# Kernel tuning notes

Hardware: AMD Instinct MI355X
Metric: run time of the kernel (lower is better)

The kernel has to match this reference:

```python
import jax, jax.numpy as jnp
import numpy as np

B, T, C, H = 8, 2048, 1024, 16
N_LAYER, LAYER_ID = 12, 1
NH = C // H           # head size = 64
CHUNK = 256


def setup_inputs() -> dict:
    key = jax.random.key(0)
    ks = jax.random.split(key, 10)
    # deterministic init matching the torch __init__
    ratio_0_to_1 = LAYER_ID / (N_LAYER - 1)
    ratio_1_to_almost0 = 1.0 - LAYER_ID / N_LAYER
    ddd = np.arange(C, dtype=np.float32) / C
    time_maa_k = (1.0 - ddd ** ratio_1_to_almost0).astype(np.float32)
    time_maa_v = (1.0 - (ddd ** ratio_1_to_almost0 + 0.3 * ratio_0_to_1)).astype(np.float32)
    time_maa_r = (1.0 - ddd ** (0.5 * ratio_1_to_almost0)).astype(np.float32)
    h_idx = np.arange(H, dtype=np.float32)
    time_decay = (-6.0 + 5.0 * (h_idx / (H - 1)) ** (0.7 + 1.3 * ratio_0_to_1)).astype(np.float32)
    s = 0.02
    return {
        "x": jax.random.normal(ks[0], (B, T, C), jnp.float32),
        "volatility": jax.random.uniform(ks[1], (B, T), jnp.float32),
        "Wvol": jax.random.normal(ks[2], (C, 1), jnp.float32) * s,
        "bvol": jnp.zeros((C,), jnp.float32),
        "time_maa_k": jnp.asarray(time_maa_k),
        "time_maa_v": jnp.asarray(time_maa_v),
        "time_maa_r": jnp.asarray(time_maa_r),
        "time_decay": jnp.asarray(time_decay),
        "Wk": jax.random.normal(ks[3], (C, C), jnp.float32) * s,
        "Wv": jax.random.normal(ks[4], (C, C), jnp.float32) * s,
        "Wr": jax.random.normal(ks[5], (C, C), jnp.float32) * s,
        "Wo": jax.random.normal(ks[6], (C, C), jnp.float32) * s,
        "gn_w": 1.0 + jax.random.normal(ks[7], (C,), jnp.float32) * s,
        "gn_b": jax.random.normal(ks[8], (C,), jnp.float32) * s,
    }


def reference(x, volatility, Wvol, bvol, time_maa_k, time_maa_v, time_maa_r,
              time_decay, Wk, Wv, Wr, Wo, gn_w, gn_b):
    b, t, c = x.shape
    h = time_decay.shape[0]
    n = c // h
    nc = t // CHUNK

    # volatility gating: sigmoid(Linear(1->C))
    v_emb = jax.nn.sigmoid(volatility[:, :, None] * Wvol[:, 0] + bvol)  # (B,T,C)
    x = x * v_emb

    # time shift (zero-pad one step at the front, drop last)
    xx = jnp.pad(x, ((0, 0), (1, 0), (0, 0)))[:, :-1] - x
    xk = x + xx * time_maa_k
    xv = x + xx * time_maa_v
    xr = x + xx * time_maa_r

    r = (xr @ Wr.T).reshape(b, t, h, n).transpose(0, 2, 1, 3)  # (B,H,T,N)
    k = (xk @ Wk.T).reshape(b, t, h, n).transpose(0, 2, 1, 3)
    v = (xv @ Wv.T).reshape(b, t, h, n).transpose(0, 2, 1, 3)

    w = jnp.exp(-jnp.exp(time_decay))[None, :, None, None]  # scalar decay per head

    # chunked linear-attention recurrence (faithful to torch loop, chunk=256, no intra-chunk mask)
    rc = r.reshape(b, h, nc, CHUNK, n).transpose(2, 0, 1, 3, 4)  # (nc,B,H,CK,N)
    kc = k.reshape(b, h, nc, CHUNK, n).transpose(2, 0, 1, 3, 4)
    vc = v.reshape(b, h, nc, CHUNK, n).transpose(2, 0, 1, 3, 4)

    def step(state, rkv):
        rr, kk, vv = rkv  # each (B,H,CK,N)
        att = jnp.einsum('bhtn,bhsn->bhts', rr, kk)            # r @ k^T
        y = w * (jnp.einsum('bhts,bhsn->bhtn', att, vv)
                 + jnp.einsum('bhtn,bhnm->bhtm', rr, state))
        new_state = w * (state + jnp.einsum('bhsn,bhsm->bhnm', kk, vv))
        return new_state, y

    state0 = jnp.zeros((b, h, n, n), x.dtype)
    _, ys = jax.lax.scan(step, state0, (rc, kc, vc))            # (nc,B,H,CK,N)
    y = ys.transpose(1, 2, 0, 3, 4).reshape(b, h, t, n)
    y = y.transpose(0, 2, 1, 3).reshape(b * t, c)

    # GroupNorm with H groups over channels
    yg = y.reshape(b * t, h, n)
    mu = yg.mean(-1, keepdims=True)
    var = yg.var(-1, keepdims=True)
    yg = (yg - mu) * jax.lax.rsqrt(var + 1e-5)
    y = (yg.reshape(b * t, c) * gn_w + gn_b).reshape(b, t, c)

    return y @ Wo.T  # dropout is identity in eval
```

## Files before the change

### kernel.cpp

```cpp
#include <hip/hip_runtime.h>

typedef unsigned short u16;
typedef __attribute__((ext_vector_type(4))) unsigned int u32x4;
typedef __attribute__((ext_vector_type(4))) float f32x4;
typedef __attribute__((ext_vector_type(8))) short s16x8;

#define B_ 8
#define T_ 2048
#define C_ 1024
#define H_ 16
#define HS_ 64
#define CHUNK_ 256
#define NC_ 8

union U8 { u32x4 u; u16 h[8]; };

__device__ __forceinline__ float b2f(u16 v) {
    union { unsigned int i; float f; } c; c.i = ((unsigned int)v) << 16; return c.f;
}
__device__ __forceinline__ u16 f2b(float f) {
    union { float f; unsigned int i; } c; c.f = f;
    unsigned int i = c.i;
    return (u16)((i + 0x7FFFu + ((i >> 16) & 1u)) >> 16);
}
__device__ __forceinline__ float fsig(float z) {
    return __builtin_amdgcn_rcpf(1.f + __expf(-z));
}

typedef __attribute__((address_space(1))) void GV;
typedef __attribute__((address_space(3))) void LV;
__device__ __forceinline__ void glds16(const void* g, void* l) {
    __builtin_amdgcn_global_load_lds((GV*)g, (LV*)l, 16, 0, 0);
}

__global__ __launch_bounds__(256) void cvt4_kernel(
    const float* __restrict__ s0, const float* __restrict__ s1,
    const float* __restrict__ s2, const float* __restrict__ s3,
    u16* __restrict__ dst)
{
    int i = blockIdx.x * 256 + threadIdx.x;
    int m = i >> 17;
    const float* s = (m == 0) ? s0 : (m == 1) ? s1 : (m == 2) ? s2 : s3;
    size_t j = (size_t)(i & 131071) * 8;
    f32x4 a = *reinterpret_cast<const f32x4*>(s + j);
    f32x4 b = *reinterpret_cast<const f32x4*>(s + j + 4);
    U8 o;
    #pragma unroll
    for (int k = 0; k < 4; k++) { o.h[k] = f2b(a[k]); o.h[4 + k] = f2b(b[k]); }
    *reinterpret_cast<u32x4*>(dst + (size_t)m * C_ * C_ + j) = o.u;
}

__global__ __launch_bounds__(256) void mix_kernel(
    const float* __restrict__ x, const float* __restrict__ vol,
    const float* __restrict__ Wvol, const float* __restrict__ bvol,
    const float* __restrict__ mk, const float* __restrict__ mv, const float* __restrict__ mr,
    u16* __restrict__ xk, u16* __restrict__ xv, u16* __restrict__ xr)
{
    int idx = blockIdx.x * 256 + threadIdx.x;
    int c0 = (idx & 127) * 8;
    int bt4 = idx >> 7;
    int t0  = (bt4 & 511) * 4;
    int b   = bt4 >> 9;
    size_t rowOff = ((size_t)b * T_ + t0) * C_ + c0;

    float wv[8], bv[8], mkv[8], mvv[8], mrv[8];
    #pragma unroll
    for (int j = 0; j < 8; j += 4) {
        f32x4 a;
        a = *reinterpret_cast<const f32x4*>(Wvol + c0 + j);
        wv[j] = a[0]; wv[j+1] = a[1]; wv[j+2] = a[2]; wv[j+3] = a[3];
        a = *reinterpret_cast<const f32x4*>(bvol + c0 + j);
        bv[j] = a[0]; bv[j+1] = a[1]; bv[j+2] = a[2]; bv[j+3] = a[3];
        a = *reinterpret_cast<const f32x4*>(mk + c0 + j);
        mkv[j] = a[0]; mkv[j+1] = a[1]; mkv[j+2] = a[2]; mkv[j+3] = a[3];
        a = *reinterpret_cast<const f32x4*>(mv + c0 + j);
        mvv[j] = a[0]; mvv[j+1] = a[1]; mvv[j+2] = a[2]; mvv[j+3] = a[3];
        a = *reinterpret_cast<const f32x4*>(mr + c0 + j);
        mrv[j] = a[0]; mrv[j+1] = a[1]; mrv[j+2] = a[2]; mrv[j+3] = a[3];
    }

    const float* volb = vol + (size_t)b * T_;
    float gp[8];
    if (t0 == 0) {
        #pragma unroll
        for (int j = 0; j < 8; j++) gp[j] = 0.f;
    } else {
        float vp = volb[t0 - 1];
        #pragma unroll
        for (int j = 0; j < 8; j += 4) {
            f32x4 a = *reinterpret_cast<const f32x4*>(x + rowOff - C_ + j);
            gp[j]   = a[0] * fsig(vp * wv[j]   + bv[j]);
            gp[j+1] = a[1] * fsig(vp * wv[j+1] + bv[j+1]);
            gp[j+2] = a[2] * fsig(vp * wv[j+2] + bv[j+2]);
            gp[j+3] = a[3] * fsig(vp * wv[j+3] + bv[j+3]);
        }
    }

    #pragma unroll
    for (int s = 0; s < 4; s++) {
        float vc = volb[t0 + s];
        size_t off = rowOff + (size_t)s * C_;
        float g[8];
        #pragma unroll
        for (int j = 0; j < 8; j += 4) {
            f32x4 a = *reinterpret_cast<const f32x4*>(x + off + j);
            g[j]   = a[0] * fsig(vc * wv[j]   + bv[j]);
            g[j+1] = a[1] * fsig(vc * wv[j+1] + bv[j+1]);
            g[j+2] = a[2] * fsig(vc * wv[j+2] + bv[j+2]);
            g[j+3] = a[3] * fsig(vc * wv[j+3] + bv[j+3]);
        }
        U8 ok, ov, orr;
        #pragma unroll
        for (int j = 0; j < 8; j++) {
            float xx = gp[j] - g[j];
            ok.h[j]  = f2b(g[j] + xx * mkv[j]);
            ov.h[j]  = f2b(g[j] + xx * mvv[j]);
            orr.h[j] = f2b(g[j] + xx * mrv[j]);
            gp[j] = g[j];
        }
        *reinterpret_cast<u32x4*>(xk + off) = ok.u;
        *reinterpret_cast<u32x4*>(xv + off) = ov.u;
        *reinterpret_cast<u32x4*>(xr + off) = orr.u;
    }
}

#define GBM_ 256
#define GBN_ 256
#define GBK_ 64
#define GK_  1024
#define GNT_ 16
#define GEMM_LDS_BYTES 131072

template<int MODE>
__global__ __launch_bounds__(512, 2) void gemm_bt(
    const u16* __restrict__ A, const u16* __restrict__ W, void* __restrict__ Cc)
{
    extern __shared__ __align__(16) u16 lds[];
    const int tid  = threadIdx.x;
    const int lane = tid & 63, w = tid >> 6;
    const int r16  = lane & 15, quad = lane >> 4;
    const int wm2  = w >> 2;
    const int wn4  = w & 3;
    const int id   = blockIdx.x;
    const int bm   = id & 63, bn = id >> 6;

    const u16* Ab = A + (size_t)bm * GBM_ * GK_;
    const u16* Wb = W + (size_t)bn * GBN_ * GK_;

    const int srow8  = lane >> 3;
    const int schunk = ((lane & 7) ^ srow8) * 8;
    const u16* aSrc  = Ab + (size_t)(w * 16 + srow8) * GK_ + schunk;
    const u16* bSrcR = Wb + (size_t)srow8 * GK_ + schunk;

    const int fA0 = (wm2 * 128 + r16) * 64;
    const int fB0 = 16384 + (wn4 * 64 + r16) * 64;
    const int c0 = ((quad)     ^ (r16 & 7)) * 8;
    const int c1 = ((quad | 4) ^ (r16 & 7)) * 8;

    const int i0_ = w * 2, i1_ = w * 2 + 1;
    const int rB0 = (i0_ >> 2) * 64 + (i0_ & 3) * 8;
    const int rB1 = (i1_ >> 2) * 64 + (i1_ & 3) * 8;

    f32x4 acc[8][4];
    #pragma unroll
    for (int mi = 0; mi < 8; mi++)
        #pragma unroll
        for (int ni = 0; ni < 4; ni++)
            acc[mi][ni] = f32x4{0.f, 0.f, 0.f, 0.f};

#define SQA(tt) do {                                                          \
    const size_t ko_ = (size_t)(tt) * 64;                                     \
    u16* db_ = lds + (((tt) & 1) * 32768) + w * 1024;                         \
    glds16(aSrc + ko_,                 db_);                                  \
    glds16(aSrc + 8   * GK_ + ko_,     db_ + 512);                            \
    glds16(aSrc + 128 * GK_ + ko_,     db_ + 8192);                           \
    glds16(aSrc + 136 * GK_ + ko_,     db_ + 8192 + 512);                     \
} while (0)

#define SQB(tt, hi) do {                                                      \
    const size_t ko_ = (size_t)(tt) * 64;                                     \
    u16* bb_ = lds + (((tt) & 1) * 32768) + 16384;                            \
    const int ra_ = rB0 + (hi) * 32, rb_ = rB1 + (hi) * 32;                   \
    glds16(bSrcR + (size_t)ra_ * GK_ + ko_, bb_ + ra_ * 64);                  \
    glds16(bSrcR + (size_t)rb_ * GK_ + ko_, bb_ + rb_ * 64);                  \
} while (0)

#define PH_BAR() do { asm volatile("" ::: "memory");                          \
    __builtin_amdgcn_s_barrier(); asm volatile("" ::: "memory"); } while (0)
#define PH_LGKM0() do { asm volatile("s_waitcnt lgkmcnt(0)" ::: "memory");    \
    __builtin_amdgcn_sched_barrier(0); } while (0)
#define LDFA(CO) { _Pragma("unroll") for (int mi = 0; mi < 8; mi++)           \
    fa[mi] = *reinterpret_cast<const s16x8*>(lds + pb + fA0 + mi * 1024 + (CO)); }
#define LDFB(NH, CO) { _Pragma("unroll") for (int ni = 0; ni < 2; ni++)       \
    fb[ni] = *reinterpret_cast<const s16x8*>(lds + pb + fB0 + ((NH) * 2 + ni) * 1024 + (CO)); }
#define MFMA16(NH) do { __builtin_amdgcn_s_setprio(1);                        \
    _Pragma("unroll") for (int mi = 0; mi < 8; mi++) {                        \
        acc[mi][(NH)*2+0] = __builtin_amdgcn_mfma_f32_16x16x32_bf16(          \
            fa[mi], fb[0], acc[mi][(NH)*2+0], 0, 0, 0);                       \
        acc[mi][(NH)*2+1] = __builtin_amdgcn_mfma_f32_16x16x32_bf16(          \
            fa[mi], fb[1], acc[mi][(NH)*2+1], 0, 0, 0);                       \
    } __builtin_amdgcn_s_setprio(0); } while (0)

    SQA(0); SQB(0, 0); SQB(0, 1);

    for (int t = 0; t < GNT_; ++t) {
        const int pb = (t & 1) * 32768;
        s16x8 fa[8], fb[2];
        asm volatile("s_waitcnt vmcnt(2)" ::: "memory");
        PH_BAR();
        LDFA(c0); LDFB(0, c0);
        if (t + 1 < GNT_) SQA(t + 1);
        PH_LGKM0(); MFMA16(0);
        if (t + 1 < GNT_) asm volatile("s_waitcnt vmcnt(4)" ::: "memory");
        else              asm volatile("s_waitcnt vmcnt(0)" ::: "memory");
        PH_BAR();
        LDFB(1, c0);
        if (t + 1 < GNT_) SQB(t + 1, 0);
        PH_LGKM0(); MFMA16(1);
        LDFA(c1); LDFB(0, c1);
        PH_BAR();
        if (t + 1 < GNT_) SQB(t + 1, 1);
        PH_LGKM0(); MFMA16(0);
        LDFB(1, c1);
        PH_BAR();
        PH_LGKM0(); MFMA16(1);
    }
#undef SQA
#undef SQB
#undef LDFA
#undef LDFB
#undef MFMA16
#undef PH_LGKM0
#undef PH_BAR

    asm volatile("s_waitcnt vmcnt(0)" ::: "memory");
    __builtin_amdgcn_s_barrier();
    asm volatile("" ::: "memory");

    if constexpr (MODE == 0) {
        float* C = (float*)Cc;
        #pragma unroll
        for (int mi = 0; mi < 8; mi++) {
            int row0 = bm * GBM_ + wm2 * 128 + mi * 16 + quad * 4;
            #pragma unroll
            for (int ni = 0; ni < 4; ni++) {
                int col = bn * GBN_ + wn4 * 64 + ni * 16 + r16;
                #pragma unroll
                for (int i = 0; i < 4; i++)
                    C[(size_t)(row0 + i) * C_ + col] = acc[mi][ni][i];
            }
        }
    } else if constexpr (MODE == 1) {
        u16* ep = lds + w * 4608;
        u16* C = (u16*)Cc;
        #pragma unroll
        for (int half = 0; half < 2; half++) {
            #pragma unroll
            for (int mi2 = 0; mi2 < 4; mi2++) {
                int mi = half * 4 + mi2;
                #pragma unroll
                for (int ni = 0; ni < 4; ni++)
                    #pragma unroll
                    for (int i = 0; i < 4; i++)
                        ep[(mi2 * 16 + quad * 4 + i) * 72 + ni * 16 + r16] =
                            f2b(acc[mi][ni][i]);
            }
            asm volatile("s_waitcnt lgkmcnt(0)" ::: "memory");
            __builtin_amdgcn_sched_barrier(0);
            #pragma unroll
            for (int it = 0; it < 8; it++) {
                int rr = it * 8 + (lane >> 3);
                u32x4 val = *reinterpret_cast<const u32x4*>(ep + rr * 72 + (lane & 7) * 8);
                size_t grow = (size_t)(bm * GBM_ + wm2 * 128 + half * 64 + rr);
                *reinterpret_cast<u32x4*>(
                    C + grow * C_ + bn * GBN_ + wn4 * 64 + (lane & 7) * 8) = val;
            }
            asm volatile("s_waitcnt vmcnt(0) lgkmcnt(0)" ::: "memory");
        }
    } else {
        u16* ep = lds + w * 8192;
        #pragma unroll
        for (int mi = 0; mi < 8; mi++) {
            const int chunk = mi * 2 + (quad >> 1);
            const int rsub = (quad & 1) * 4;
            #pragma unroll
            for (int ni = 0; ni < 4; ni++) {
                const int col = ni * 16 + r16;
                u16* p = ep + col * 128 + ((chunk ^ col) & 15) * 8 + rsub;
                p[0] = f2b(acc[mi][ni][0]);
                p[1] = f2b(acc[mi][ni][1]);
                p[2] = f2b(acc[mi][ni][2]);
                p[3] = f2b(acc[mi][ni][3]);
            }
        }
        asm volatile("s_waitcnt lgkmcnt(0)" ::: "memory");
        __builtin_amdgcn_sched_barrier(0);
        u16* C = (u16*)Cc;
        const int cl = lane >> 2, ch4 = lane & 3;
        const int gc0 = bn * 16 + wn4 * 4;
        const int tt0 = bm * 8 + wm2 * 4;
        #pragma unroll
        for (int it = 0; it < 16; it++) {
            const int col_l = (it & 3) * 16 + cl;
            const int chunk = (it >> 2) * 4 + ch4;
            u32x4 val = *reinterpret_cast<const u32x4*>(
                ep + col_l * 128 + ((chunk ^ col_l) & 15) * 8);
            const size_t tile = (size_t)(gc0 + (it & 3)) * 512 + tt0 + (it >> 2);
            *reinterpret_cast<u32x4*>(C + tile * 512 + cl * 32 + ch4 * 8) = val;
        }
    }
}

#define KVS_LDS_BYTES 98304

__global__ __launch_bounds__(512) void kvscan_kernel(
    const u16* __restrict__ kT, const u16* __restrict__ vT,
    const float* __restrict__ td, u16* __restrict__ stT)
{
    extern __shared__ __align__(16) u16 klds[];
    const int bm2 = blockIdx.x;
    const int mh = bm2 & 1, bh = bm2 >> 1;
    const int h = bh & (H_ - 1), b = bh >> 4;
    const float wdec = expf(-expf(td[h]));
    const int tid = threadIdx.x, lane = tid & 63, w = tid >> 6;
    const int r16 = lane & 15, quad = lane >> 4;
    const int cgn = w >> 1;
    const int ck  = w & 1;
    const int tt0 = b * 64;
    const int loff = r16 * 32 + quad * 8;

#define KSTG(jj, bb) do {                                                     \
    u16* db_ = klds + (bb) * 24576;                                           \
    _Pragma("unroll")                                                         \
    for (int q = 0; q < 6; q++) {                                             \
        const int tau = w * 6 + q;                                            \
        const u16* src;                                                       \
        if (tau < 32)                                                         \
            src = vT + ((size_t)(h * 4 + (tau >> 3)) * 512 +                  \
                        tt0 + (jj) * 8 + (tau & 7)) * 512;                    \
        else                                                                  \
            src = kT + ((size_t)(h * 4 + mh * 2 + ((tau - 32) >> 3)) * 512 +  \
                        tt0 + (jj) * 8 + ((tau - 32) & 7)) * 512;             \
        glds16(src + (size_t)lane * 8, db_ + tau * 512);                      \
    }                                                                         \
} while (0)

    KSTG(0, 0);

    f32x4 st = f32x4{0.f, 0.f, 0.f, 0.f};
    for (int j = 0; j < NC_; ++j) {
        asm volatile("s_waitcnt vmcnt(0)" ::: "memory");
        __syncthreads();
        if (j + 1 < NC_) KSTG(j + 1, (j + 1) & 1);
        const u16* bb = klds + (j & 1) * 24576;
        f32x4 acc = f32x4{0.f, 0.f, 0.f, 0.f};
        #pragma unroll
        for (int ks = 0; ks < 8; ks++) {
            s16x8 fa = *reinterpret_cast<const s16x8*>(
                bb + (cgn * 8 + ks) * 512 + loff);
            s16x8 fb = *reinterpret_cast<const s16x8*>(
                bb + (32 + ck * 8 + ks) * 512 + loff);
            acc = __builtin_amdgcn_mfma_f32_16x16x32_bf16(fa, fb, acc, 0, 0, 0);
        }
        st = (st + acc) * wdec;
        u16* out = stT + ((size_t)bh * NC_ + j) * 4096;
        #pragma unroll
        for (int i = 0; i < 4; i++)
            out[(cgn * 16 + quad * 4 + i) * HS_ + mh * 32 + ck * 16 + r16] =
                f2b(st[i]);
    }
#undef KSTG
}

__global__ __launch_bounds__(256) void rstate_gn_kernel(
    const u16* __restrict__ r, const u16* __restrict__ stT,
    const float* __restrict__ gnw, const float* __restrict__ gnb, u16* __restrict__ ygn)
{
    int blk = blockIdx.x;
    int c  = blk & (NC_ - 1);
    int bh = blk >> 3;
    int h = bh & (H_ - 1);
    int b = bh >> 4;
    __shared__ __align__(16) u16 sT[HS_ * 72];
    int tid = threadIdx.x, lane = tid & 63, wave = tid >> 6;
    int r16 = lane & 15, quad = lane >> 4;

    const u16* sg = stT + (size_t)blk * (HS_ * HS_);
    for (int i = tid; i < 512; i += 256) {
        int n = i >> 3, c8 = (i & 7) * 8;
        *reinterpret_cast<u32x4*>(&sT[n * 72 + c8]) =
            *reinterpret_cast<const u32x4*>(sg + n * HS_ + c8);
    }
    __syncthreads();

    size_t rowBase = (size_t)(b * T_ + c * CHUNK_ + wave * 64);
    f32x4 acc[4][4];
    #pragma unroll
    for (int mi = 0; mi < 4; mi++)
        #pragma unroll
        for (int ni = 0; ni < 4; ni++)
            acc[mi][ni] = f32x4{0.f, 0.f, 0.f, 0.f};

    #pragma unroll
    for (int ks = 0; ks < 2; ks++) {
        int kb = ks * 32 + quad * 8;
        s16x8 fa[4], fb[4];
        #pragma unroll
        for (int mi = 0; mi < 4; mi++)
            fa[mi] = *reinterpret_cast<const s16x8*>(
                r + (rowBase + mi * 16 + r16) * C_ + h * HS_ + kb);
        #pragma unroll
        for (int ni = 0; ni < 4; ni++)
            fb[ni] = *reinterpret_cast<const s16x8*>(&sT[(ni * 16 + r16) * 72 + kb]);
        #pragma unroll
        for (int mi = 0; mi < 4; mi++)
            #pragma unroll
            for (int ni = 0; ni < 4; ni++)
                acc[mi][ni] = __builtin_amdgcn_mfma_f32_16x16x32_bf16(fa[mi], fb[ni], acc[mi][ni], 0, 0, 0);
    }

    float gwv[4], gbv[4];
    #pragma unroll
    for (int ni = 0; ni < 4; ni++) {
        int col = ni * 16 + r16;
        gwv[ni] = gnw[h * HS_ + col];
        gbv[ni] = gnb[h * HS_ + col];
    }
    #pragma unroll
    for (int mi = 0; mi < 4; mi++) {
        float s1[4], s2[4];
        #pragma unroll
        for (int i = 0; i < 4; i++) {
            float s = 0.f, ss = 0.f;
            #pragma unroll
            for (int ni = 0; ni < 4; ni++) {
                float v = acc[mi][ni][i];
                s += v; ss += v * v;
            }
            s1[i] = s; s2[i] = ss;
        }
        #pragma unroll
        for (int d = 1; d < 16; d <<= 1) {
            #pragma unroll
            for (int i = 0; i < 4; i++) {
                s1[i] += __shfl_xor(s1[i], d);
                s2[i] += __shfl_xor(s2[i], d);
            }
        }
        #pragma unroll
        for (int i = 0; i < 4; i++) {
            float mu = s1[i] * (1.f / 64.f);
            float var = s2[i] * (1.f / 64.f) - mu * mu;
            float sc = rsqrtf(var + 1e-5f);
            size_t ob = (rowBase + mi * 16 + quad * 4 + i) * C_ + h * HS_;
            #pragma unroll
            for (int ni = 0; ni < 4; ni++)
                ygn[ob + ni * 16 + r16] = f2b((acc[mi][ni][i] - mu) * sc * gwv[ni] + gbv[ni]);
        }
    }
}

extern "C" void kernel_launch(void* const* d_in, const int* in_sizes, int n_in,
                              void* d_out, int out_size, void* d_ws, size_t ws_size,
                              hipStream_t stream) {
    const float* x    = (const float*)d_in[0];
    const float* vol  = (const float*)d_in[1];
    const float* Wvol = (const float*)d_in[2];
    const float* bvol = (const float*)d_in[3];
    const float* mk   = (const float*)d_in[4];
    const float* mv   = (const float*)d_in[5];
    const float* mr   = (const float*)d_in[6];
    const float* td   = (const float*)d_in[7];
    const float* Wk   = (const float*)d_in[8];
    const float* Wv   = (const float*)d_in[9];
    const float* Wr   = (const float*)d_in[10];
    const float* Wo   = (const float*)d_in[11];
    const float* gnw  = (const float*)d_in[12];
    const float* gnb  = (const float*)d_in[13];
    float* out = (float*)d_out;

    static bool init_attr = []() {
        hipFuncSetAttribute(reinterpret_cast<const void*>(gemm_bt<0>),
                            hipFuncAttributeMaxDynamicSharedMemorySize, GEMM_LDS_BYTES);
        hipFuncSetAttribute(reinterpret_cast<const void*>(gemm_bt<1>),
                            hipFuncAttributeMaxDynamicSharedMemorySize, GEMM_LDS_BYTES);
        hipFuncSetAttribute(reinterpret_cast<const void*>(gemm_bt<2>),
                            hipFuncAttributeMaxDynamicSharedMemorySize, GEMM_LDS_BYTES);
        hipFuncSetAttribute(reinterpret_cast<const void*>(kvscan_kernel),
                            hipFuncAttributeMaxDynamicSharedMemorySize, KVS_LDS_BYTES);
        return true;
    }();
    (void)init_attr;

    char* ws = (char*)d_ws;
    const size_t SLOT = (size_t)B_ * T_ * C_ * 2;
    u16* xr = (u16*)(ws + 0 * SLOT);
    u16* xk = (u16*)(ws + 1 * SLOT);
    u16* xv = (u16*)(ws + 2 * SLOT);
    u16* rb = (u16*)(ws + 3 * SLOT);
    u16* kbT = (u16*)(ws + 0 * SLOT);
    u16* vbT = (u16*)(ws + 1 * SLOT);
    u16* stT = (u16*)(ws + 2 * SLOT + SLOT / 2);
    u16* ygn = (u16*)(ws + 0 * SLOT);
    u16* wtb = (u16*)(ws + 4 * SLOT);
    u16* wrb = wtb;
    u16* wkb = wrb + (size_t)C_ * C_;
    u16* wvb = wkb + (size_t)C_ * C_;
    u16* wob = wvb + (size_t)C_ * C_;

    cvt4_kernel<<<dim3(4 * (C_ * C_ / 8) / 256), dim3(256), 0, stream>>>(Wr, Wk, Wv, Wo, wtb);

    mix_kernel<<<dim3(2048), dim3(256), 0, stream>>>(
        x, vol, Wvol, bvol, mk, mv, mr, xk, xv, xr);

    gemm_bt<1><<<dim3(256), dim3(512), GEMM_LDS_BYTES, stream>>>(xr, wrb, rb);
    gemm_bt<2><<<dim3(256), dim3(512), GEMM_LDS_BYTES, stream>>>(xk, wkb, kbT);
    gemm_bt<2><<<dim3(256), dim3(512), GEMM_LDS_BYTES, stream>>>(xv, wvb, vbT);

    kvscan_kernel<<<dim3(B_ * H_ * 2), dim3(512), KVS_LDS_BYTES, stream>>>(kbT, vbT, td, stT);

    rstate_gn_kernel<<<dim3(B_ * H_ * NC_), dim3(256), 0, stream>>>(rb, stT, gnw, gnb, ygn);

    gemm_bt<0><<<dim3(256), dim3(512), GEMM_LDS_BYTES, stream>>>(ygn, wob, out);
}
```

Before: 329.5 us.

## Merge weight conversion with mixing, batch three projection GEMMs, triple-buffer kvscan

The weight bf16 conversion now runs as extra blocks of the token-mix kernel, so one launch replaces two. The r/k/v projection GEMMs are merged into a single 768-block launch through a shared device core function, which removes launch gaps and the tail under-utilisation of three separate 256-block grids. The kv-scan kernel moves from double to triple buffering with a partial vmcnt wait, so loads stay two chunks ahead. This costs more LDS in kvscan, which may lower occupancy, and adds a branch to the prep kernel.

```diff
diff --git a/kernel.cpp b/kernel.cpp
--- a/kernel.cpp
+++ b/kernel.cpp
@@ -33,29 +33,28 @@
     __builtin_amdgcn_global_load_lds((GV*)g, (LV*)l, 16, 0, 0);
 }
 
-__global__ __launch_bounds__(256) void cvt4_kernel(
-    const float* __restrict__ s0, const float* __restrict__ s1,
-    const float* __restrict__ s2, const float* __restrict__ s3,
-    u16* __restrict__ dst)
-{
-    int i = blockIdx.x * 256 + threadIdx.x;
-    int m = i >> 17;
-    const float* s = (m == 0) ? s0 : (m == 1) ? s1 : (m == 2) ? s2 : s3;
-    size_t j = (size_t)(i & 131071) * 8;
-    f32x4 a = *reinterpret_cast<const f32x4*>(s + j);
-    f32x4 b = *reinterpret_cast<const f32x4*>(s + j + 4);
-    U8 o;
-    #pragma unroll
-    for (int k = 0; k < 4; k++) { o.h[k] = f2b(a[k]); o.h[4 + k] = f2b(b[k]); }
-    *reinterpret_cast<u32x4*>(dst + (size_t)m * C_ * C_ + j) = o.u;
-}
-
-__global__ __launch_bounds__(256) void mix_kernel(
+__global__ __launch_bounds__(256) void prep_kernel(
     const float* __restrict__ x, const float* __restrict__ vol,
     const float* __restrict__ Wvol, const float* __restrict__ bvol,
     const float* __restrict__ mk, const float* __restrict__ mv, const float* __restrict__ mr,
-    u16* __restrict__ xk, u16* __restrict__ xv, u16* __restrict__ xr)
+    u16* __restrict__ xk, u16* __restrict__ xv, u16* __restrict__ xr,
+    const float* __restrict__ s0, const float* __restrict__ s1,
+    const float* __restrict__ s2, const float* __restrict__ s3,
+    u16* __restrict__ wdst)
 {
+    if (blockIdx.x >= 2048) {
+        int i = (blockIdx.x - 2048) * 256 + threadIdx.x;
+        int m = i >> 17;
+        const float* s = (m == 0) ? s0 : (m == 1) ? s1 : (m == 2) ? s2 : s3;
+        size_t j = (size_t)(i & 131071) * 8;
+        f32x4 a = *reinterpret_cast<const f32x4*>(s + j);
+        f32x4 b = *reinterpret_cast<const f32x4*>(s + j + 4);
+        U8 o;
+        #pragma unroll
+        for (int k = 0; k < 4; k++) { o.h[k] = f2b(a[k]); o.h[4 + k] = f2b(b[k]); }
+        *reinterpret_cast<u32x4*>(wdst + (size_t)m * C_ * C_ + j) = o.u;
+        return;
+    }
     int idx = blockIdx.x * 256 + threadIdx.x;
     int c0 = (idx & 127) * 8;
     int bt4 = idx >> 7;
@@ -132,16 +131,15 @@
 #define GEMM_LDS_BYTES 131072
 
 template<int MODE>
-__global__ __launch_bounds__(512, 2) void gemm_bt(
-    const u16* __restrict__ A, const u16* __restrict__ W, void* __restrict__ Cc)
+__device__ __forceinline__ void gemm_core(
+    u16* lds, const u16* __restrict__ A, const u16* __restrict__ W,
+    void* __restrict__ Cc, const int id)
 {
-    extern __shared__ __align__(16) u16 lds[];
     const int tid  = threadIdx.x;
     const int lane = tid & 63, w = tid >> 6;
     const int r16  = lane & 15, quad = lane >> 4;
     const int wm2  = w >> 2;
     const int wn4  = w & 3;
-    const int id   = blockIdx.x;
     const int bm   = id & 63, bn = id >> 6;
 
     const u16* Ab = A + (size_t)bm * GBM_ * GK_;
@@ -311,7 +309,27 @@
     }
 }
 
-#define KVS_LDS_BYTES 98304
+__global__ __launch_bounds__(512, 2) void gemm3_kernel(
+    const u16* __restrict__ xr, const u16* __restrict__ xk, const u16* __restrict__ xv,
+    const u16* __restrict__ wtb, u16* __restrict__ rb,
+    u16* __restrict__ kbT, u16* __restrict__ vbT)
+{
+    extern __shared__ __align__(16) u16 lds[];
+    const int id = blockIdx.x;
+    const int seg = id >> 8, lid = id & 255;
+    if (seg == 0)      gemm_core<1>(lds, xr, wtb,           rb,  lid);
+    else if (seg == 1) gemm_core<2>(lds, xk, wtb + 1048576, kbT, lid);
+    else               gemm_core<2>(lds, xv, wtb + 2097152, vbT, lid);
+}
+
+__global__ __launch_bounds__(512, 2) void gemm_out_kernel(
+    const u16* __restrict__ ygn, const u16* __restrict__ wob, float* __restrict__ out)
+{
+    extern __shared__ __align__(16) u16 lds[];
+    gemm_core<0>(lds, ygn, wob, out, blockIdx.x);
+}
+
+#define KVS_LDS_BYTES 147456
 
 __global__ __launch_bounds__(512) void kvscan_kernel(
     const u16* __restrict__ kT, const u16* __restrict__ vT,
@@ -329,8 +347,8 @@
     const int tt0 = b * 64;
     const int loff = r16 * 32 + quad * 8;
 
-#define KSTG(jj, bb) do {                                                     \
-    u16* db_ = klds + (bb) * 24576;                                           \
+#define KSTG(jj) do {                                                         \
+    u16* db_ = klds + ((jj) % 3) * 24576;                                     \
     _Pragma("unroll")                                                         \
     for (int q = 0; q < 6; q++) {                                             \
         const int tau = w * 6 + q;                                            \
@@ -345,14 +363,18 @@
     }                                                                         \
 } while (0)
 
-    KSTG(0, 0);
+    KSTG(0);
+    KSTG(1);
 
     f32x4 st = f32x4{0.f, 0.f, 0.f, 0.f};
     for (int j = 0; j < NC_; ++j) {
-        asm volatile("s_waitcnt vmcnt(0)" ::: "memory");
-        __syncthreads();
-        if (j + 1 < NC_) KSTG(j + 1, (j + 1) & 1);
-        const u16* bb = klds + (j & 1) * 24576;
+        if (j + 1 < NC_) asm volatile("s_waitcnt vmcnt(6)" ::: "memory");
+        else             asm volatile("s_waitcnt vmcnt(0)" ::: "memory");
+        asm volatile("" ::: "memory");
+        __builtin_amdgcn_s_barrier();
+        asm volatile("" ::: "memory");
+        if (j + 2 < NC_) KSTG(j + 2);
+        const u16* bb = klds + (j % 3) * 24576;
         f32x4 acc = f32x4{0.f, 0.f, 0.f, 0.f};
         #pragma unroll
         for (int ks = 0; ks < 8; ks++) {
@@ -480,11 +502,9 @@
     float* out = (float*)d_out;
 
     static bool init_attr = []() {
-        hipFuncSetAttribute(reinterpret_cast<const void*>(gemm_bt<0>),
+        hipFuncSetAttribute(reinterpret_cast<const void*>(gemm3_kernel),
                             hipFuncAttributeMaxDynamicSharedMemorySize, GEMM_LDS_BYTES);
-        hipFuncSetAttribute(reinterpret_cast<const void*>(gemm_bt<1>),
-                            hipFuncAttributeMaxDynamicSharedMemorySize, GEMM_LDS_BYTES);
-        hipFuncSetAttribute(reinterpret_cast<const void*>(gemm_bt<2>),
+        hipFuncSetAttribute(reinterpret_cast<const void*>(gemm_out_kernel),
                             hipFuncAttributeMaxDynamicSharedMemorySize, GEMM_LDS_BYTES);
         hipFuncSetAttribute(reinterpret_cast<const void*>(kvscan_kernel),
                             hipFuncAttributeMaxDynamicSharedMemorySize, KVS_LDS_BYTES);
@@ -503,23 +523,17 @@
     u16* stT = (u16*)(ws + 2 * SLOT + SLOT / 2);
     u16* ygn = (u16*)(ws + 0 * SLOT);
     u16* wtb = (u16*)(ws + 4 * SLOT);
-    u16* wrb = wtb;
-    u16* wkb = wrb + (size_t)C_ * C_;
-    u16* wvb = wkb + (size_t)C_ * C_;
-    u16* wob = wvb + (size_t)C_ * C_;
-
-    cvt4_kernel<<<dim3(4 * (C_ * C_ / 8) / 256), dim3(256), 0, stream>>>(Wr, Wk, Wv, Wo, wtb);
-
-    mix_kernel<<<dim3(2048), dim3(256), 0, stream>>>(
-        x, vol, Wvol, bvol, mk, mv, mr, xk, xv, xr);
-
-    gemm_bt<1><<<dim3(256), dim3(512), GEMM_LDS_BYTES, stream>>>(xr, wrb, rb);
-    gemm_bt<2><<<dim3(256), dim3(512), GEMM_LDS_BYTES, stream>>>(xk, wkb, kbT);
-    gemm_bt<2><<<dim3(256), dim3(512), GEMM_LDS_BYTES, stream>>>(xv, wvb, vbT);
+    u16* wob = wtb + (size_t)3 * C_ * C_;
+
+    prep_kernel<<<dim3(4096), dim3(256), 0, stream>>>(
+        x, vol, Wvol, bvol, mk, mv, mr, xk, xv, xr, Wr, Wk, Wv, Wo, wtb);
+
+    gemm3_kernel<<<dim3(768), dim3(512), GEMM_LDS_BYTES, stream>>>(
+        xr, xk, xv, wtb, rb, kbT, vbT);
 
     kvscan_kernel<<<dim3(B_ * H_ * 2), dim3(512), KVS_LDS_BYTES, stream>>>(kbT, vbT, td, stT);
 
     rstate_gn_kernel<<<dim3(B_ * H_ * NC_), dim3(256), 0, stream>>>(rb, stT, gnw, gnb, ygn);
 
-    gemm_bt<0><<<dim3(256), dim3(512), GEMM_LDS_BYTES, stream>>>(ygn, wob, out);
-}
+    gemm_out_kernel<<<dim3(256), dim3(512), GEMM_LDS_BYTES, stream>>>(ygn, wob, out);
+}
```

Result: faster. 312.6 us (-5.2%).
